# Performance work log

Measured on AMD Instinct MI355X. Metric: run time of the kernel, lower is better.

The kernel has to match this reference:

```python
import jax, jax.numpy as jnp
import numpy as np
from jax import lax

K1, K2, DATA_RANGE = 0.01, 0.03, 1.0
MS_WEIGHTS = np.array([0.0448, 0.2856, 0.3001, 0.2363, 0.1333], dtype=np.float32)


def _gauss1d(size, sigma):
    coords = jnp.arange(size, dtype=jnp.float32) - size // 2
    g = jnp.exp(-(coords ** 2) / (2.0 * sigma ** 2))
    return g / jnp.sum(g)


def _gaussian_blur(x, win1d):
    # separable depthwise gaussian blur, VALID padding (matches pytorch-msssim)
    C = x.shape[1]
    size = win1d.shape[0]
    kh = jnp.tile(win1d.reshape(1, 1, size, 1), (C, 1, 1, 1))  # (C,1,k,1)
    kw = jnp.tile(win1d.reshape(1, 1, 1, size), (C, 1, 1, 1))  # (C,1,1,k)
    dn = ('NCHW', 'OIHW', 'NCHW')
    x = lax.conv_general_dilated(x, kh, (1, 1), 'VALID',
                                 dimension_numbers=dn, feature_group_count=C)
    x = lax.conv_general_dilated(x, kw, (1, 1), 'VALID',
                                 dimension_numbers=dn, feature_group_count=C)
    return x


def _ssim_per_channel(X, Y, win1d):
    C1 = (K1 * DATA_RANGE) ** 2
    C2 = (K2 * DATA_RANGE) ** 2
    mu1 = _gaussian_blur(X, win1d)
    mu2 = _gaussian_blur(Y, win1d)
    mu1_sq, mu2_sq, mu1_mu2 = mu1 * mu1, mu2 * mu2, mu1 * mu2
    sigma1_sq = _gaussian_blur(X * X, win1d) - mu1_sq
    sigma2_sq = _gaussian_blur(Y * Y, win1d) - mu2_sq
    sigma12 = _gaussian_blur(X * Y, win1d) - mu1_mu2
    cs_map = (2.0 * sigma12 + C2) / (sigma1_sq + sigma2_sq + C2)
    ssim_map = ((2.0 * mu1_mu2 + C1) / (mu1_sq + mu2_sq + C1)) * cs_map
    return ssim_map.mean(axis=(2, 3)), cs_map.mean(axis=(2, 3))  # (B,C) each


def _avg_pool2(x, ph, pw):
    # F.avg_pool2d(kernel=2, stride=2, padding=(ph,pw), count_include_pad=True)
    s = lax.reduce_window(x, 0.0, lax.add, (1, 1, 2, 2), (1, 1, 2, 2),
                          ((0, 0), (0, 0), (ph, ph), (pw, pw)))
    return s * 0.25


def _ms_ssim(gen, gt):
    weights = jnp.asarray(MS_WEIGHTS)
    win_size = 3 if gen.shape[3] < 256 else 11
    win1d = _gauss1d(win_size, 1.5)
    levels = weights.shape[0]
    mcs = []
    for i in range(levels):
        ssim_pc, cs = _ssim_per_channel(gen, gt, win1d)
        if i < levels - 1:
            mcs.append(jax.nn.relu(cs))
            ph, pw = gen.shape[2] % 2, gen.shape[3] % 2
            gen = _avg_pool2(gen, ph, pw)
            gt = _avg_pool2(gt, ph, pw)
    ssim_pc = jax.nn.relu(ssim_pc)
    mcs_and_ssim = jnp.stack(mcs + [ssim_pc], axis=0)  # (levels,B,C)
    ms_ssim_val = jnp.prod(mcs_and_ssim ** weights[:, None, None], axis=0)
    return ms_ssim_val.mean()


def setup_inputs() -> dict:
    key = jax.random.key(0)
    k1, k2 = jax.random.split(key)
    gen_frames = jax.random.uniform(k1, (16, 3, 512, 512), dtype=jnp.float32)
    gt_frames = jax.random.uniform(k2, (16, 3, 512, 512), dtype=jnp.float32)
    return {"gen_frames": gen_frames, "gt_frames": gt_frames}


def reference(gen_frames, gt_frames):
    return 1.0 - _ms_ssim(gen_frames, gt_frames)
```

## Files before the change

### kernel.cpp

```cpp
#include <hip/hip_runtime.h>


#define TW 32
#define TH 128
#define RPT 16
#define HALO 10
#define IW (TW + HALO)
#define IH (TH + HALO)
#define ISTR (IW + 1)

__device__ __constant__ float G11[11] = {
    0.001028380f, 0.007598758f, 0.036000773f, 0.109360680f, 0.213005529f,
    0.266011731f,
    0.213005529f, 0.109360680f, 0.036000773f, 0.007598758f, 0.001028380f
};

__device__ __forceinline__ float fastdiv(float a, float b) {
    float r = __builtin_amdgcn_rcpf(b);
    r = r * __builtin_fmaf(-b, r, 2.0f);
    return a * r;
}

#define HBLUR(ROW, SLOT) do {                                              \
    const float2* pxy_ = &sxy[(ROW) * ISTR + tx];                          \
    float bx_ = 0.f, by_ = 0.f, bxx_ = 0.f, byy_ = 0.f, bxy_ = 0.f;        \
    _Pragma("unroll")                                                      \
    for (int t_ = 0; t_ < 11; ++t_) {                                      \
        float w_  = G11[t_];                                               \
        float2 v_ = pxy_[t_];                                              \
        float wx_ = w_ * v_.x;                                             \
        float wy_ = w_ * v_.y;                                             \
        bx_  += wx_;                                                       \
        by_  += wy_;                                                       \
        bxx_ = __builtin_fmaf(wx_, v_.x, bxx_);                            \
        byy_ = __builtin_fmaf(wy_, v_.y, byy_);                            \
        bxy_ = __builtin_fmaf(wx_, v_.y, bxy_);                            \
    }                                                                      \
    rbx[(SLOT)] = bx_; rby[(SLOT)] = by_; rbxx[(SLOT)] = bxx_;             \
    rbyy[(SLOT)] = byy_; rbxy[(SLOT)] = bxy_;                              \
} while (0)

#define VTAP(I, T) do {                                                    \
    const float w_ = G11[(T)];                                             \
    m1  = __builtin_fmaf(w_, rbx [((I)+(T)) % 11], m1);                    \
    m2  = __builtin_fmaf(w_, rby [((I)+(T)) % 11], m2);                    \
    qxx = __builtin_fmaf(w_, rbxx[((I)+(T)) % 11], qxx);                   \
    qyy = __builtin_fmaf(w_, rbyy[((I)+(T)) % 11], qyy);                   \
    qxy = __builtin_fmaf(w_, rbxy[((I)+(T)) % 11], qxy);                   \
} while (0)

#define STEP(I) do {                                                       \
    HBLUR(g0 + 10 + (I), (10 + (I)) % 11);                                 \
    float m1 = 0.f, m2 = 0.f, qxx = 0.f, qyy = 0.f, qxy = 0.f;             \
    VTAP(I,0); VTAP(I,1); VTAP(I,2); VTAP(I,3); VTAP(I,4); VTAP(I,5);      \
    VTAP(I,6); VTAP(I,7); VTAP(I,8); VTAP(I,9); VTAP(I,10);                \
    if (colok && (oy + g0 + (I)) < Hs) {                                   \
        const float C1 = 0.0001f, C2 = 0.0009f;                            \
        float mu1s = m1 * m1, mu2s = m2 * m2, mu12 = m1 * m2;              \
        float s1  = qxx - mu1s;                                            \
        float s2  = qyy - mu2s;                                            \
        float s12 = qxy - mu12;                                            \
        float cs  = fastdiv(2.f * s12 + C2, s1 + s2 + C2);                 \
        float ss  = fastdiv((2.f * mu12 + C1) * cs, mu1s + mu2s + C1);     \
        ssum += ss;                                                        \
        csum += cs;                                                        \
    }                                                                      \
} while (0)

__global__ __launch_bounds__(256)
void ssim_level_kernel(const float* __restrict__ X, const float* __restrict__ Y,
                       int H, int W, int Hs, int Ws, float* __restrict__ acc)
{
    __shared__ float2 sxy[IH * ISTR];
    __shared__ float red[2][4];

    const int bc  = blockIdx.z;
    const int ox  = blockIdx.x * TW;
    const int oy  = blockIdx.y * TH;
    const int tid = threadIdx.x;
    const size_t base = (size_t)bc * H * W;

    for (int idx = tid; idx < IH * IW; idx += 256) {
        int r = idx / IW;
        int c = idx - r * IW;
        int gr = oy + r; if (gr > H - 1) gr = H - 1;
        int gc = ox + c; if (gc > W - 1) gc = W - 1;
        size_t g = base + (size_t)gr * W + gc;
        sxy[r * ISTR + c] = make_float2(X[g], Y[g]);
    }
    __syncthreads();

    const int tx = tid & 31;
    const int ty = tid >> 5;
    const int g0 = ty * RPT;

    float rbx[11], rby[11], rbxx[11], rbyy[11], rbxy[11];

    HBLUR(g0 + 0, 0); HBLUR(g0 + 1, 1); HBLUR(g0 + 2, 2); HBLUR(g0 + 3, 3);
    HBLUR(g0 + 4, 4); HBLUR(g0 + 5, 5); HBLUR(g0 + 6, 6); HBLUR(g0 + 7, 7);
    HBLUR(g0 + 8, 8); HBLUR(g0 + 9, 9);

    const bool colok = (ox + tx) < Ws;
    float ssum = 0.f, csum = 0.f;

    STEP(0);  STEP(1);  STEP(2);  STEP(3);
    STEP(4);  STEP(5);  STEP(6);  STEP(7);
    STEP(8);  STEP(9);  STEP(10); STEP(11);
    STEP(12); STEP(13); STEP(14); STEP(15);

#pragma unroll
    for (int off = 32; off; off >>= 1) {
        ssum += __shfl_down(ssum, off);
        csum += __shfl_down(csum, off);
    }
    if ((tid & 63) == 0) {
        red[0][tid >> 6] = ssum;
        red[1][tid >> 6] = csum;
    }
    __syncthreads();
    if (tid == 0) {
        float s = red[0][0] + red[0][1] + red[0][2] + red[0][3];
        float c = red[1][0] + red[1][1] + red[1][2] + red[1][3];
        atomicAdd(&acc[bc * 2 + 0], s);
        atomicAdd(&acc[bc * 2 + 1], c);
    }
}

__launch_bounds__(256)
__global__ void down_kernel(const float* __restrict__ Xi, const float* __restrict__ Yi,
                            float* __restrict__ Xo, float* __restrict__ Yo,
                            int Ho, int Wo, int n)
{
    int idx = blockIdx.x * 256 + threadIdx.x;
    if (idx >= n) return;
    int w  = idx % Wo;
    int t  = idx / Wo;
    int h  = t % Ho;
    int bc = t / Ho;
    int W  = Wo * 2;
    size_t ib = (size_t)bc * (4 * Ho * Wo) + (size_t)(2 * h) * W + 2 * w;
    float2 a0 = *reinterpret_cast<const float2*>(Xi + ib);
    float2 a1 = *reinterpret_cast<const float2*>(Xi + ib + W);
    Xo[idx] = 0.25f * (a0.x + a0.y + a1.x + a1.y);
    float2 b0 = *reinterpret_cast<const float2*>(Yi + ib);
    float2 b1 = *reinterpret_cast<const float2*>(Yi + ib + W);
    Yo[idx] = 0.25f * (b0.x + b0.y + b1.x + b1.y);
}

__launch_bounds__(64)
__global__ void finalize_kernel(const float* __restrict__ acc, float* __restrict__ out)
{
    const int lane = threadIdx.x;
    float prod = 0.f;
    if (lane < 48) {
        const float npix[5] = {252004.f, 60516.f, 13924.f, 2916.f, 484.f};
        const float wgt[5]  = {0.0448f, 0.2856f, 0.3001f, 0.2363f, 0.1333f};
        prod = 1.f;
#pragma unroll
        for (int l = 0; l < 5; ++l) {
            float v = (l < 4) ? acc[l * 96 + lane * 2 + 1] : acc[l * 96 + lane * 2 + 0];
            v = v / npix[l];
            v = fmaxf(v, 0.f);
            prod *= powf(v, wgt[l]);
        }
    }
#pragma unroll
    for (int off = 32; off; off >>= 1) prod += __shfl_down(prod, off);
    if (lane == 0) out[0] = 1.f - prod / 48.f;
}

extern "C" void kernel_launch(void* const* d_in, const int* in_sizes, int n_in,
                              void* d_out, int out_size, void* d_ws, size_t ws_size,
                              hipStream_t stream)
{
    const float* gen = (const float*)d_in[0];
    const float* gt  = (const float*)d_in[1];
    float* out = (float*)d_out;

    char* ws = (char*)d_ws;
    float* acc = (float*)ws;
    float* p   = (float*)(ws + 2048);
    float* g1 = p; p += (size_t)48 * 256 * 256;
    float* t1 = p; p += (size_t)48 * 256 * 256;
    float* g2 = p; p += (size_t)48 * 128 * 128;
    float* t2 = p; p += (size_t)48 * 128 * 128;
    float* g3 = p; p += (size_t)48 * 64 * 64;
    float* t3 = p; p += (size_t)48 * 64 * 64;
    float* g4 = p; p += (size_t)48 * 32 * 32;
    float* t4 = p; p += (size_t)48 * 32 * 32;

    hipMemsetAsync(acc, 0, 5 * 48 * 2 * sizeof(float), stream);

    auto launch_ssim = [&](const float* X, const float* Y, int H, int lvl) {
        int Hs = H - 10;
        dim3 grid((Hs + TW - 1) / TW, (Hs + TH - 1) / TH, 48);
        ssim_level_kernel<<<grid, 256, 0, stream>>>(X, Y, H, H, Hs, Hs, acc + lvl * 96);
    };
    auto launch_down = [&](const float* Xi, const float* Yi, float* Xo, float* Yo, int Ho) {
        int n = 48 * Ho * Ho;
        down_kernel<<<(n + 255) / 256, 256, 0, stream>>>(Xi, Yi, Xo, Yo, Ho, Ho, n);
    };

    launch_ssim(gen, gt, 512, 0);
    launch_down(gen, gt, g1, t1, 256);
    launch_ssim(g1, t1, 256, 1);
    launch_down(g1, t1, g2, t2, 128);
    launch_ssim(g2, t2, 128, 2);
    launch_down(g2, t2, g3, t3, 64);
    launch_ssim(g3, t3, 64, 3);
    launch_down(g3, t3, g4, t4, 32);
    launch_ssim(g4, t4, 32, 4);
    finalize_kernel<<<1, 64, 0, stream>>>(acc, out);
}
```

Baseline: 341.6 us.

## Fuse 2x2 average pooling into the SSIM tile kernel and drop down_kernel

Each SSIM block now writes the 2x2 pooled next-level image straight from its shared-memory tile, so the separate downsample kernels that re-read the full inputs from global memory are gone. The tile height is halved from 128 to 64 rows so one 256-thread block maps exactly onto the 32x64 pooled region. Tile loads now use float2 global reads. The shorter tile raises the halo overhead and the repeated horizontal-blur work per output row.

```diff
diff --git a/kernel.cpp b/kernel.cpp
--- a/kernel.cpp
+++ b/kernel.cpp
@@ -2,8 +2,8 @@
 
 
 #define TW 32
-#define TH 128
-#define RPT 16
+#define TH 64
+#define RPT 8
 #define HALO 10
 #define IW (TW + HALO)
 #define IH (TH + HALO)
@@ -69,7 +69,9 @@
 
 __global__ __launch_bounds__(256)
 void ssim_level_kernel(const float* __restrict__ X, const float* __restrict__ Y,
-                       int H, int W, int Hs, int Ws, float* __restrict__ acc)
+                       int H, int W, int Hs, int Ws, float* __restrict__ acc,
+                       float* __restrict__ Xo, float* __restrict__ Yo,
+                       int Wp, int do_pool)
 {
     __shared__ float2 sxy[IH * ISTR];
     __shared__ float red[2][4];
@@ -80,13 +82,17 @@
     const int tid = threadIdx.x;
     const size_t base = (size_t)bc * H * W;
 
-    for (int idx = tid; idx < IH * IW; idx += 256) {
-        int r = idx / IW;
-        int c = idx - r * IW;
-        int gr = oy + r; if (gr > H - 1) gr = H - 1;
-        int gc = ox + c; if (gc > W - 1) gc = W - 1;
+    for (int p = tid; p < IH * 21; p += 256) {
+        int r  = p / 21;
+        int c2 = p - r * 21;
+        int gr = oy + r;      if (gr > H - 1) gr = H - 1;
+        int gc = ox + 2 * c2; if (gc > W - 2) gc = W - 2;
         size_t g = base + (size_t)gr * W + gc;
-        sxy[r * ISTR + c] = make_float2(X[g], Y[g]);
+        float2 xv = *reinterpret_cast<const float2*>(X + g);
+        float2 yv = *reinterpret_cast<const float2*>(Y + g);
+        float2* dst = &sxy[r * ISTR + 2 * c2];
+        dst[0] = make_float2(xv.x, yv.x);
+        dst[1] = make_float2(xv.y, yv.y);
     }
     __syncthreads();
 
@@ -103,10 +109,25 @@
     const bool colok = (ox + tx) < Ws;
     float ssum = 0.f, csum = 0.f;
 
-    STEP(0);  STEP(1);  STEP(2);  STEP(3);
-    STEP(4);  STEP(5);  STEP(6);  STEP(7);
-    STEP(8);  STEP(9);  STEP(10); STEP(11);
-    STEP(12); STEP(13); STEP(14); STEP(15);
+    STEP(0); STEP(1); STEP(2); STEP(3);
+    STEP(4); STEP(5); STEP(6); STEP(7);
+
+    if (do_pool) {
+        int i  = tid >> 3;
+        int j0 = (tid & 7) * 2;
+        const float2* r0 = &sxy[(2 * i)     * ISTR + 2 * j0];
+        const float2* r1 = &sxy[(2 * i + 1) * ISTR + 2 * j0];
+        float2 a0 = r0[0], a1 = r0[1], b0 = r1[0], b1 = r1[1];
+        float2 c0 = r0[2], c1 = r0[3], d0 = r1[2], d1 = r1[3];
+        float2 xo, yo;
+        xo.x = 0.25f * (a0.x + a1.x + b0.x + b1.x);
+        yo.x = 0.25f * (a0.y + a1.y + b0.y + b1.y);
+        xo.y = 0.25f * (c0.x + c1.x + d0.x + d1.x);
+        yo.y = 0.25f * (c0.y + c1.y + d0.y + d1.y);
+        size_t po = (size_t)bc * Wp * Wp + (size_t)((oy >> 1) + i) * Wp + (ox >> 1) + j0;
+        *reinterpret_cast<float2*>(Xo + po) = xo;
+        *reinterpret_cast<float2*>(Yo + po) = yo;
+    }
 
 #pragma unroll
     for (int off = 32; off; off >>= 1) {
@@ -124,27 +145,6 @@
         atomicAdd(&acc[bc * 2 + 0], s);
         atomicAdd(&acc[bc * 2 + 1], c);
     }
-}
-
-__launch_bounds__(256)
-__global__ void down_kernel(const float* __restrict__ Xi, const float* __restrict__ Yi,
-                            float* __restrict__ Xo, float* __restrict__ Yo,
-                            int Ho, int Wo, int n)
-{
-    int idx = blockIdx.x * 256 + threadIdx.x;
-    if (idx >= n) return;
-    int w  = idx % Wo;
-    int t  = idx / Wo;
-    int h  = t % Ho;
-    int bc = t / Ho;
-    int W  = Wo * 2;
-    size_t ib = (size_t)bc * (4 * Ho * Wo) + (size_t)(2 * h) * W + 2 * w;
-    float2 a0 = *reinterpret_cast<const float2*>(Xi + ib);
-    float2 a1 = *reinterpret_cast<const float2*>(Xi + ib + W);
-    Xo[idx] = 0.25f * (a0.x + a0.y + a1.x + a1.y);
-    float2 b0 = *reinterpret_cast<const float2*>(Yi + ib);
-    float2 b1 = *reinterpret_cast<const float2*>(Yi + ib + W);
-    Yo[idx] = 0.25f * (b0.x + b0.y + b1.x + b1.y);
 }
 
 __launch_bounds__(64)
@@ -191,24 +191,19 @@
 
     hipMemsetAsync(acc, 0, 5 * 48 * 2 * sizeof(float), stream);
 
-    auto launch_ssim = [&](const float* X, const float* Y, int H, int lvl) {
+    auto launch_ssim = [&](const float* X, const float* Y, int H, int lvl,
+                           float* Xo, float* Yo) {
         int Hs = H - 10;
         dim3 grid((Hs + TW - 1) / TW, (Hs + TH - 1) / TH, 48);
-        ssim_level_kernel<<<grid, 256, 0, stream>>>(X, Y, H, H, Hs, Hs, acc + lvl * 96);
+        ssim_level_kernel<<<grid, 256, 0, stream>>>(X, Y, H, H, Hs, Hs,
+                                                    acc + lvl * 96,
+                                                    Xo, Yo, H / 2, Xo != nullptr);
     };
-    auto launch_down = [&](const float* Xi, const float* Yi, float* Xo, float* Yo, int Ho) {
-        int n = 48 * Ho * Ho;
-        down_kernel<<<(n + 255) / 256, 256, 0, stream>>>(Xi, Yi, Xo, Yo, Ho, Ho, n);
-    };
-
-    launch_ssim(gen, gt, 512, 0);
-    launch_down(gen, gt, g1, t1, 256);
-    launch_ssim(g1, t1, 256, 1);
-    launch_down(g1, t1, g2, t2, 128);
-    launch_ssim(g2, t2, 128, 2);
-    launch_down(g2, t2, g3, t3, 64);
-    launch_ssim(g3, t3, 64, 3);
-    launch_down(g3, t3, g4, t4, 32);
-    launch_ssim(g4, t4, 32, 4);
+
+    launch_ssim(gen, gt, 512, 0, g1, t1);
+    launch_ssim(g1, t1, 256, 1, g2, t2);
+    launch_ssim(g2, t2, 128, 2, g3, t3);
+    launch_ssim(g3, t3, 64, 3, g4, t4);
+    launch_ssim(g4, t4, 32, 4, nullptr, nullptr);
     finalize_kernel<<<1, 64, 0, stream>>>(acc, out);
 }
```

After: 283.7 us. 16.9% less time.
